# Performance work log

Hardware: AMD Instinct MI355X
Metric: run time of the kernel (lower is better)

The kernel has to match this reference:

```python
import jax, jax.numpy as jnp
import numpy as np

B, C, H, W = 2, 256, 96, 192
GROUPS = 4
K = 9  # search_window_1d = (1, 9) -> 9 candidates, x-offsets -4..4, y-offset 0


def bilinear_sample(img, coords):
    """F.grid_sample(mode='bilinear', padding_mode='zeros', align_corners=True)
    with absolute pixel coordinates (torchvision optical-flow grid_sample wrapper:
    normalize by 2*x/(W-1)-1 then grid_sample align_corners=True == identity mapping).
    img: [B, C, H, W]; coords: [B, Hg, Wg, 2] as (x, y). Returns [B, C, Hg, Wg]."""
    Bi, Ci, Hi, Wi = img.shape
    x = coords[..., 0]
    y = coords[..., 1]
    x0 = jnp.floor(x)
    y0 = jnp.floor(y)
    wx1 = x - x0
    wy1 = y - y0
    wx0 = 1.0 - wx1
    wy0 = 1.0 - wy1
    flat = img.reshape(Bi, Ci, Hi * Wi)

    def gather(ix, iy):
        valid = (ix >= 0) & (ix <= Wi - 1) & (iy >= 0) & (iy <= Hi - 1)
        ixc = jnp.clip(ix, 0, Wi - 1).astype(jnp.int32)
        iyc = jnp.clip(iy, 0, Hi - 1).astype(jnp.int32)
        idx = (iyc * Wi + ixc).reshape(Bi, 1, -1)  # [B,1,Hg*Wg]
        g = jnp.take_along_axis(flat, idx, axis=2)  # [B,C,Hg*Wg]
        g = g.reshape(Bi, Ci, *ix.shape[1:])
        return g * valid[:, None].astype(img.dtype)

    out = (gather(x0, y0) * (wx0 * wy0)[:, None]
           + gather(x0 + 1, y0) * (wx1 * wy0)[:, None]
           + gather(x0, y0 + 1) * (wx0 * wy1)[:, None]
           + gather(x0 + 1, y0 + 1) * (wx1 * wy1)[:, None])
    return out


def setup_inputs() -> dict:
    key = jax.random.key(0)
    k1, k2, k3, k4 = jax.random.split(key, 4)
    return {
        "left_feature": jax.random.normal(k1, (B, C, H, W), dtype=jnp.float32),
        "right_feature": jax.random.normal(k2, (B, C, H, W), dtype=jnp.float32),
        "flow": jax.random.normal(k3, (B, 2, H, W), dtype=jnp.float32),
        "extra_offset": jax.random.normal(k4, (B, 2 * K, H, W), dtype=jnp.float32),
    }


def reference(left_feature, right_feature, flow, extra_offset):
    Bf, Cf, Hf, Wf = left_feature.shape
    gc = Cf // GROUPS
    dt = left_feature.dtype
    # 1d window offsets: meshgrid(arange(-4,5), arange(0,1), 'xy') -> (x, 0) pairs
    xs = jnp.arange(-4, 5, dtype=dt)
    win_offs = jnp.stack([xs, jnp.zeros_like(xs)], axis=-1)  # [K,2] (x,y)
    # extra_offset: [B, K, 2, H, W] -> [B, K, H, W, 2]
    extra = extra_offset.reshape(Bf, K, 2, Hf, Wf).transpose(0, 1, 3, 4, 2)
    offsets = win_offs[None, :, None, None, :] + extra  # [B,K,H,W,2]
    # base coords grid (x, y) + flow
    yy, xx = jnp.meshgrid(jnp.arange(Hf), jnp.arange(Wf), indexing="ij")
    base = jnp.stack([xx, yy], axis=-1).astype(dt)  # [H,W,2]
    coords = base[None] + flow.transpose(0, 2, 3, 1)  # [B,H,W,2]
    coords = coords[:, None] + offsets  # [B,K,H,W,2]
    coords = coords.reshape(Bf, K * Hf, Wf, 2)
    # All groups share identical window/dilation -> sample full right feature once.
    sampled = bilinear_sample(right_feature, coords)  # [B,C,K*H,W]
    sampled = sampled.reshape(Bf, GROUPS, gc, K, Hf, Wf)
    left = left_feature.reshape(Bf, GROUPS, gc, 1, Hf, Wf)
    corr = jnp.mean(left * sampled, axis=2)  # [B,G,K,H,W]
    return corr.reshape(Bf, GROUPS * K, Hf, Wf)
```

## Files before the change

### kernel.cpp

```cpp
#include <hip/hip_runtime.h>


namespace {
constexpr int kB = 2;
constexpr int kC = 256;
constexpr int kH = 96;
constexpr int kW = 192;
constexpr int kG = 4;
constexpr int kGC = kC / kG;
constexpr int kK = 9;
constexpr int kHW = kH * kW;
constexpr size_t kPlane = (size_t)kC * kHW;
constexpr int kTransBlocks = (kHW / 64) * (kC / 64) * kB;
constexpr int kPx = 16;
constexpr int kCorrBlocks  = kB * kHW / kPx;
}

typedef _Float16 half8_t __attribute__((ext_vector_type(8)));
typedef _Float16 half2_t __attribute__((ext_vector_type(2)));

struct TapMeta {
  int4   off;
  float4 wgt;
};

__device__ __forceinline__ float dot8(half8_t a, half8_t b, float acc) {
#if __has_builtin(__builtin_amdgcn_fdot2)
  #pragma unroll
  for (int i = 0; i < 4; ++i) {
    half2_t a2 = {a[2 * i], a[2 * i + 1]};
    half2_t b2 = {b[2 * i], b[2 * i + 1]};
    acc = __builtin_amdgcn_fdot2(a2, b2, acc, false);
  }
#else
  #pragma unroll
  for (int i = 0; i < 8; ++i) acc += (float)a[i] * (float)b[i];
#endif
  return acc;
}

__device__ __forceinline__ half8_t ld16(const _Float16* p) {
  half8_t r;
  asm volatile("global_load_dwordx4 %0, %1, off"
               : "=&v"(r) : "v"(p));
  return r;
}

__global__ __launch_bounds__(256) void prepass_kernel(
    const float* __restrict__ right, _Float16* __restrict__ right_t)
{
  __shared__ float tile[64][65];
  int tb = blockIdx.x;
  int pt = tb % (kHW / 64);
  int ct = (tb / (kHW / 64)) % 4;
  int b  = tb / ((kHW / 64) * 4);
  int p0 = pt * 64, c0 = ct * 64;
  const float* inb = right + (size_t)b * kPlane;
  _Float16*   outb = right_t + (size_t)b * kPlane;
  int t = threadIdx.x;
  int cl = t >> 2;
  int q  = t & 3;
  #pragma unroll
  for (int i = 0; i < 4; ++i) {
    int j = q + 4 * i;
    float4 v = *(const float4*)(inb + (size_t)(c0 + cl) * kHW + p0 + 4 * j);
    tile[cl][4 * j + 0] = v.x;
    tile[cl][4 * j + 1] = v.y;
    tile[cl][4 * j + 2] = v.z;
    tile[cl][4 * j + 3] = v.w;
  }
  __syncthreads();
  int pl8 = t >> 3;
  int c8  = t & 7;
  #pragma unroll
  for (int i = 0; i < 2; ++i) {
    int px = pl8 + 32 * i;
    half8_t hv;
    #pragma unroll
    for (int j = 0; j < 8; ++j)
      hv[j] = (_Float16)tile[8 * c8 + j][px];
    *(half8_t*)(outb + (size_t)(p0 + px) * kC + c0 + 8 * c8) = hv;
  }
}

__global__ __launch_bounds__(512, 2) void corr_fp16_kernel(
    const _Float16* __restrict__ right_t, const float* __restrict__ left,
    const float* __restrict__ flow, const float* __restrict__ extra,
    float* __restrict__ out)
{
  __shared__ _Float16 smleft[kPx][kC];
  __shared__ float    smflow[20][kPx];
  __shared__ TapMeta  smeta[kPx * kK];
  __shared__ float    smout[kG * kK][kPx];

  int sb = (blockIdx.x & 7) * (kCorrBlocks / 8) + (blockIdx.x >> 3);
  int blockPix = sb * kPx;
  int b    = blockPix / kHW;
  int pix0 = blockPix % kHW;

  int t = threadIdx.x;

  #pragma unroll
  for (int it = 0; it < 2; ++it) {
    int c = (t >> 2) + 128 * it;
    int q = t & 3;
    float4 v = *(const float4*)(left + (size_t)b * kPlane +
                                (size_t)c * kHW + pix0 + 4 * q);
    smleft[4 * q + 0][c] = (_Float16)v.x;
    smleft[4 * q + 1][c] = (_Float16)v.y;
    smleft[4 * q + 2][c] = (_Float16)v.z;
    smleft[4 * q + 3][c] = (_Float16)v.w;
  }

  if (t < 320) {
    int fr = t >> 4, fpx = t & 15;
    const float* src = (fr < 2)
        ? flow  + ((size_t)b * 2  + fr)       * kHW + pix0 + fpx
        : extra + ((size_t)b * 18 + (fr - 2)) * kHW + pix0 + fpx;
    smflow[fr][fpx] = *src;
  }
  __syncthreads();

  if (t < kPx * kK) {
    int px = t / kK;
    int k  = t - px * kK;
    int gpix = pix0 + px;
    int w = gpix % kW, h = gpix / kW;

    float bx = (float)w + smflow[0][px];
    float by = (float)h + smflow[1][px];
    float xx = bx + (float)(k - 4) + smflow[2 + 2 * k][px];
    float yy = by + smflow[2 + 2 * k + 1][px];
    float xf = floorf(xx), yf = floorf(yy);
    float fx = xx - xf, fy = yy - yf;
    int ix0 = (int)xf, iy0 = (int)yf;
    int ix1 = ix0 + 1, iy1 = iy0 + 1;
    bool vx0 = (ix0 >= 0) && (ix0 < kW);
    bool vx1 = (ix1 >= 0) && (ix1 < kW);
    bool vy0 = (iy0 >= 0) && (iy0 < kH);
    bool vy1 = (iy1 >= 0) && (iy1 < kH);
    int xc0 = min(max(ix0, 0), kW - 1);
    int xc1 = min(max(ix1, 0), kW - 1);
    int yc0 = min(max(iy0, 0), kH - 1);
    int yc1 = min(max(iy1, 0), kH - 1);
    float wx0 = 1.f - fx, wy0 = 1.f - fy;
    TapMeta m;
    m.off.x = (yc0 * kW + xc0) * kC;
    m.off.y = (yc0 * kW + xc1) * kC;
    m.off.z = (yc1 * kW + xc0) * kC;
    m.off.w = (yc1 * kW + xc1) * kC;
    m.wgt.x = wx0 * wy0 * ((vx0 && vy0) ? 1.f : 0.f);
    m.wgt.y = fx  * wy0 * ((vx1 && vy0) ? 1.f : 0.f);
    m.wgt.z = wx0 * fy  * ((vx0 && vy1) ? 1.f : 0.f);
    m.wgt.w = fx  * fy  * ((vx1 && vy1) ? 1.f : 0.f);
    smeta[t] = m;
  }

  int wv   = t >> 6;
  int lane = t & 63;
  int p    = lane >> 5;
  int cl   = lane & 31;
  int px   = wv * 2 + p;

  const _Float16* Rb = right_t + (size_t)b * kPlane + cl * 8;

  __syncthreads();

  half8_t l8 = *(const half8_t*)&smleft[px][cl * 8];
  const TapMeta* mp = smeta + px * kK;

  float rr[kK];
  half8_t tA[12], tB[12], tC[12];

#define ISSUE_TAPS(T, KB) do {                                           \
    int4 o0 = mp[(KB)].off, o1 = mp[(KB) + 1].off, o2 = mp[(KB) + 2].off; \
    T[0]  = ld16(Rb + o0.x);                                             \
    T[1]  = ld16(Rb + o0.y);                                             \
    T[2]  = ld16(Rb + o0.z);                                             \
    T[3]  = ld16(Rb + o0.w);                                             \
    T[4]  = ld16(Rb + o1.x);                                             \
    T[5]  = ld16(Rb + o1.y);                                             \
    T[6]  = ld16(Rb + o1.z);                                             \
    T[7]  = ld16(Rb + o1.w);                                             \
    T[8]  = ld16(Rb + o2.x);                                             \
    T[9]  = ld16(Rb + o2.y);                                             \
    T[10] = ld16(Rb + o2.z);                                             \
    T[11] = ld16(Rb + o2.w);                                             \
  } while (0)

#define COMP_TAPS(T, KB) do {                                      \
    _Pragma("unroll")                                              \
    for (int j = 0; j < 3; ++j) {                                  \
      float4 w4 = mp[(KB) + j].wgt;                                \
      float d00 = dot8(T[4 * j + 0], l8, 0.f);                     \
      float d01 = dot8(T[4 * j + 1], l8, 0.f);                     \
      float d10 = dot8(T[4 * j + 2], l8, 0.f);                     \
      float d11 = dot8(T[4 * j + 3], l8, 0.f);                     \
      float r = w4.x * d00 + w4.y * d01 + w4.z * d10 + w4.w * d11; \
      r += __shfl_xor(r, 1);                                       \
      r += __shfl_xor(r, 2);                                       \
      r += __shfl_xor(r, 4);                                       \
      rr[(KB) + j] = r;                                            \
    }                                                              \
  } while (0)

  ISSUE_TAPS(tA, 0);
  ISSUE_TAPS(tB, 3);
  asm volatile("s_waitcnt vmcnt(12)" ::: "memory");
  __builtin_amdgcn_sched_barrier(0);
  COMP_TAPS(tA, 0);
  ISSUE_TAPS(tC, 6);
  asm volatile("s_waitcnt vmcnt(12)" ::: "memory");
  __builtin_amdgcn_sched_barrier(0);
  COMP_TAPS(tB, 3);
  asm volatile("s_waitcnt vmcnt(0)" ::: "memory");
  __builtin_amdgcn_sched_barrier(0);
  COMP_TAPS(tC, 6);

#undef ISSUE_TAPS
#undef COMP_TAPS

  if ((cl & 7) == 0) {
    int g = cl >> 3;
    #pragma unroll
    for (int k = 0; k < kK; ++k)
      smout[g * kK + k][px] = rr[k] * (1.f / kGC);
  }
  __syncthreads();
  {
    float* ob = out + (size_t)b * kG * kK * kHW + pix0;
    int r   = t >> 4;
    int px2 = t & 15;
    ob[(size_t)r * kHW + px2] = smout[r][px2];
    if (t < (kG * kK - 32) * kPx) {
      int r2 = 32 + (t >> 4);
      ob[(size_t)r2 * kHW + px2] = smout[r2][px2];
    }
  }
}

__global__ __launch_bounds__(256) void crestereo_corr_fallback(
    const float* __restrict__ left, const float* __restrict__ right,
    const float* __restrict__ flow, const float* __restrict__ extra,
    float* __restrict__ out)
{
  int t = blockIdx.x * blockDim.x + threadIdx.x;
  int w = t % kW;
  int h = (t / kW) % kH;
  int k = (t / kHW) % kK;
  int g = (t / (kHW * kK)) % kG;
  int b = t / (kHW * kK * kG);

  int pix = h * kW + w;
  const float* flowb = flow + b * 2 * kHW + pix;
  float x = (float)(w + (k - 4)) + flowb[0];
  float y = (float)h + flowb[kHW];
  const float* extb = extra + (size_t)(b * 2 * kK + 2 * k) * kHW + pix;
  x += extb[0];
  y += extb[kHW];

  float xf = floorf(x), yf = floorf(y);
  float fx = x - xf, fy = y - yf;
  int ix0 = (int)xf, iy0 = (int)yf;
  int ix1 = ix0 + 1, iy1 = iy0 + 1;
  bool vx0 = (ix0 >= 0) && (ix0 < kW);
  bool vx1 = (ix1 >= 0) && (ix1 < kW);
  bool vy0 = (iy0 >= 0) && (iy0 < kH);
  bool vy1 = (iy1 >= 0) && (iy1 < kH);
  int xc0 = min(max(ix0, 0), kW - 1);
  int xc1 = min(max(ix1, 0), kW - 1);
  int yc0 = min(max(iy0, 0), kH - 1);
  int yc1 = min(max(iy1, 0), kH - 1);
  float wx0 = 1.f - fx, wy0 = 1.f - fy;
  float w00 = wx0 * wy0 * ((vx0 && vy0) ? 1.f : 0.f);
  float w01 = fx  * wy0 * ((vx1 && vy0) ? 1.f : 0.f);
  float w10 = wx0 * fy  * ((vx0 && vy1) ? 1.f : 0.f);
  float w11 = fx  * fy  * ((vx1 && vy1) ? 1.f : 0.f);
  int idx = yc0 * kW + xc0;
  int dx  = xc1 - xc0;
  int dyw = (yc1 - yc0) * kW;

  const float* Rb = right + (size_t)(b * kC + g * kGC) * kHW + idx;
  const float* Lb = left  + (size_t)(b * kC + g * kGC) * kHW + pix;

  float acc = 0.f;
  #pragma unroll 4
  for (int c = 0; c < kGC; ++c) {
    const float* Rc = Rb + (size_t)c * kHW;
    float l   = Lb[(size_t)c * kHW];
    acc += l * (w00 * Rc[0] + w01 * Rc[dx] + w10 * Rc[dyw] + w11 * Rc[dx + dyw]);
  }
  out[(size_t)((b * kG + g) * kK + k) * kHW + pix] = acc * (1.f / kGC);
}

extern "C" void kernel_launch(void* const* d_in, const int* in_sizes, int n_in,
                              void* d_out, int out_size, void* d_ws, size_t ws_size,
                              hipStream_t stream) {
  const float* left  = (const float*)d_in[0];
  const float* right = (const float*)d_in[1];
  const float* flow  = (const float*)d_in[2];
  const float* extra = (const float*)d_in[3];
  float* out = (float*)d_out;

  size_t t_bytes = (size_t)kB * kPlane * sizeof(_Float16);
  if (ws_size >= t_bytes) {
    _Float16* right_t = (_Float16*)d_ws;

    prepass_kernel<<<kTransBlocks, 256, 0, stream>>>(right, right_t);
    corr_fp16_kernel<<<kCorrBlocks, 512, 0, stream>>>(
        right_t, left, flow, extra, out);
  } else {
    int total = kB * kG * kK * kH * kW;
    crestereo_corr_fallback<<<(total + 255) / 256, 256, 0, stream>>>(
        left, right, flow, extra, out);
  }
}
```

Measured before the change: 134.6 us.

## Halve pixels per block, drop LDS staging of flow and output

```diff
diff --git a/kernel.cpp b/kernel.cpp
--- a/kernel.cpp
+++ b/kernel.cpp
@@ -12,7 +12,7 @@
 constexpr int kHW = kH * kW;
 constexpr size_t kPlane = (size_t)kC * kHW;
 constexpr int kTransBlocks = (kHW / 64) * (kC / 64) * kB;
-constexpr int kPx = 16;
+constexpr int kPx = 8;
 constexpr int kCorrBlocks  = kB * kHW / kPx;
 }
 
@@ -83,15 +83,13 @@
   }
 }
 
-__global__ __launch_bounds__(512, 2) void corr_fp16_kernel(
+__global__ __launch_bounds__(256, 4) void corr_fp16_kernel(
     const _Float16* __restrict__ right_t, const float* __restrict__ left,
     const float* __restrict__ flow, const float* __restrict__ extra,
     float* __restrict__ out)
 {
+  __shared__ TapMeta  smeta[kPx * kK];
   __shared__ _Float16 smleft[kPx][kC];
-  __shared__ float    smflow[20][kPx];
-  __shared__ TapMeta  smeta[kPx * kK];
-  __shared__ float    smout[kG * kK][kPx];
 
   int sb = (blockIdx.x & 7) * (kCorrBlocks / 8) + (blockIdx.x >> 3);
   int blockPix = sb * kPx;
@@ -102,8 +100,8 @@
 
   #pragma unroll
   for (int it = 0; it < 2; ++it) {
-    int c = (t >> 2) + 128 * it;
-    int q = t & 3;
+    int c = (t >> 1) + 128 * it;
+    int q = t & 1;
     float4 v = *(const float4*)(left + (size_t)b * kPlane +
                                 (size_t)c * kHW + pix0 + 4 * q);
     smleft[4 * q + 0][c] = (_Float16)v.x;
@@ -112,25 +110,19 @@
     smleft[4 * q + 3][c] = (_Float16)v.w;
   }
 
-  if (t < 320) {
-    int fr = t >> 4, fpx = t & 15;
-    const float* src = (fr < 2)
-        ? flow  + ((size_t)b * 2  + fr)       * kHW + pix0 + fpx
-        : extra + ((size_t)b * 18 + (fr - 2)) * kHW + pix0 + fpx;
-    smflow[fr][fpx] = *src;
-  }
-  __syncthreads();
-
   if (t < kPx * kK) {
     int px = t / kK;
     int k  = t - px * kK;
     int gpix = pix0 + px;
     int w = gpix % kW, h = gpix / kW;
 
-    float bx = (float)w + smflow[0][px];
-    float by = (float)h + smflow[1][px];
-    float xx = bx + (float)(k - 4) + smflow[2 + 2 * k][px];
-    float yy = by + smflow[2 + 2 * k + 1][px];
+    const float* flowb = flow + (size_t)b * 2 * kHW + gpix;
+    float bx = (float)w + flowb[0];
+    float by = (float)h + flowb[kHW];
+    const float* extb = extra + (size_t)b * 2 * kK * kHW + gpix;
+
+    float xx = bx + (float)(k - 4) + extb[(size_t)(2 * k) * kHW];
+    float yy = by + extb[(size_t)(2 * k + 1) * kHW];
     float xf = floorf(xx), yf = floorf(yy);
     float fx = xx - xf, fy = yy - yf;
     int ix0 = (int)xf, iy0 = (int)yf;
@@ -161,6 +153,7 @@
   int p    = lane >> 5;
   int cl   = lane & 31;
   int px   = wv * 2 + p;
+  int pix  = pix0 + px;
 
   const _Float16* Rb = right_t + (size_t)b * kPlane + cl * 8;
 
@@ -220,22 +213,12 @@
 #undef ISSUE_TAPS
 #undef COMP_TAPS
 
+  int g = cl >> 3;
   if ((cl & 7) == 0) {
-    int g = cl >> 3;
+    float* outp = out + ((size_t)b * kG + g) * kK * kHW + pix;
     #pragma unroll
     for (int k = 0; k < kK; ++k)
-      smout[g * kK + k][px] = rr[k] * (1.f / kGC);
-  }
-  __syncthreads();
-  {
-    float* ob = out + (size_t)b * kG * kK * kHW + pix0;
-    int r   = t >> 4;
-    int px2 = t & 15;
-    ob[(size_t)r * kHW + px2] = smout[r][px2];
-    if (t < (kG * kK - 32) * kPx) {
-      int r2 = 32 + (t >> 4);
-      ob[(size_t)r2 * kHW + px2] = smout[r2][px2];
-    }
+      outp[(size_t)k * kHW] = rr[k] * (1.f / kGC);
   }
 }
 
@@ -307,7 +290,7 @@
     _Float16* right_t = (_Float16*)d_ws;
 
     prepass_kernel<<<kTransBlocks, 256, 0, stream>>>(right, right_t);
-    corr_fp16_kernel<<<kCorrBlocks, 512, 0, stream>>>(
+    corr_fp16_kernel<<<kCorrBlocks, 256, 0, stream>>>(
         right_t, left, flow, extra, out);
   } else {
     int total = kB * kG * kK * kH * kW;
```

After: 138.8 us. 1.03x slower.
